# Performance work log

Hardware: AMD Instinct MI355X
Metric: run time of the kernel (lower is better)

## Reference

```python
import jax, jax.numpy as jnp
import numpy as np

N = 2048      # nodes
E = 65536     # edges (avg degree 32)
D_I = 64      # input feature dim
D_O = 64      # output feature dim
EPS = 1e-6


def _one_hot_incidence(key, n, e):
    # each edge column has a single 1 at its endpoint node row -> [N, E]
    idx = jax.random.randint(key, (e,), 0, n)
    return jnp.zeros((n, e), jnp.float32).at[idx, jnp.arange(e)].set(1.0)


def setup_inputs() -> dict:
    key = jax.random.key(0)
    k_x, k_s, k_t, k_wf, k_ww = jax.random.split(key, 5)
    x = jax.random.normal(k_x, (N, D_I), jnp.float32)
    src = _one_hot_incidence(k_s, N, E)
    tgt = _one_hot_incidence(k_t, N, E)
    # xavier-uniform init for Linear(2*d_i, d_o) and Linear(2*d_i, 1)
    lim_f = float(np.sqrt(6.0 / (2 * D_I + D_O)))
    lim_w = float(np.sqrt(6.0 / (2 * D_I + 1)))
    W_f = jax.random.uniform(k_wf, (2 * D_I, D_O), jnp.float32, -lim_f, lim_f)
    b_f = jnp.zeros((D_O,), jnp.float32)
    W_w = jax.random.uniform(k_ww, (2 * D_I, 1), jnp.float32, -lim_w, lim_w)
    b_w = jnp.zeros((1,), jnp.float32)
    return {"x": x, "src": src, "tgt": tgt,
            "W_f": W_f, "b_f": b_f, "W_w": W_w, "b_w": b_w}


def reference(x, src, tgt, W_f, b_f, W_w, b_w):
    # gather source/target node features per edge via dense one-hot matmuls
    hsrc = src.T @ x                      # [E, d_i]
    htgt = tgt.T @ x                      # [E, d_i]
    h = jnp.concatenate([hsrc, htgt], axis=1)   # [E, 2*d_i]
    y = jax.nn.relu(h @ W_f + b_f)        # [E, d_o]
    a = h @ W_w + b_w                     # [E, 1]
    a_max = jnp.mean(a, axis=0, keepdims=True)
    a_exp = jnp.exp(a - a_max)            # [E, 1]
    a_sum = tgt @ a_exp                   # [N, 1] segment-sum over edges per target node
    a_tgt = tgt.T @ a_sum                 # [E, 1] broadcast denominators back to edges
    a_att = a_exp / (a_tgt + EPS)         # edge softmax weights
    o = tgt @ (y * a_att)                 # [N, d_o] weighted scatter-sum
    return o
```

## Files before the change

kernel.cpp:

```cpp
#include <hip/hip_runtime.h>
#include <hip/hip_bf16.h>

#define N_NODES 2048
#define N_EDGES 65536
#define D_IN    64
#define D_OUT   64
#define GAT_EPS 1e-6f

typedef unsigned short u16;
typedef unsigned int   u32;
typedef __attribute__((ext_vector_type(8))) short frag8;
typedef __attribute__((ext_vector_type(4))) float f32x4;

__device__ __forceinline__ u16 f2bf(float f) {
    union { u32 u; float f; } x; x.f = f;
    u32 lsb = (x.u >> 16) & 1u;
    x.u += 0x7fffu + lsb;
    return (u16)(x.u >> 16);
}

__global__ void k_zero2(float* __restrict__ a, int na, float* __restrict__ b, int nb) {
    int i = blockIdx.x * 256 + threadIdx.x;
    if (i < na) a[i] = 0.0f;
    else if (i - na < nb) b[i - na] = 0.0f;
}

__global__ void k_extract2(const uint4* __restrict__ src, const uint4* __restrict__ tgt,
                           int* __restrict__ sidx, int* __restrict__ tidx) {
    u32 b = blockIdx.x;
    const uint4* m; int* idx;
    if (b < 131072u) { m = src; idx = sidx; }
    else             { m = tgt; idx = tidx; b -= 131072u; }
    u32 t = b * 256u + threadIdx.x;
    uint4 v = m[t];
    if (v.x | v.y | v.z | v.w) {
        u32 elem = t * 4u;
        int n = (int)(elem >> 16);
        int e = (int)(elem & 65535u);
        if (v.x) idx[e]     = n;
        if (v.y) idx[e + 1] = n;
        if (v.z) idx[e + 2] = n;
        if (v.w) idx[e + 3] = n;
    }
}

__global__ void k_edge_score(const float* __restrict__ x,
                             const int* __restrict__ sidx, const int* __restrict__ tidx,
                             const float* __restrict__ Ww, const float* __restrict__ bw,
                             float* __restrict__ a, float* __restrict__ mean_acc) {
    __shared__ float ww[2 * D_IN];
    int tid = threadIdx.x;
    if (tid < 2 * D_IN) ww[tid] = Ww[tid];
    __syncthreads();
    int e = blockIdx.x * 256 + tid;
    int s = sidx[e] & (N_NODES - 1);
    int t = tidx[e] & (N_NODES - 1);
    const float4* xs = (const float4*)(x + s * D_IN);
    const float4* xt = (const float4*)(x + t * D_IN);
    float sum = bw[0];
    #pragma unroll
    for (int i = 0; i < 16; ++i) {
        float4 v = xs[i];
        sum += v.x * ww[i * 4] + v.y * ww[i * 4 + 1]
             + v.z * ww[i * 4 + 2] + v.w * ww[i * 4 + 3];
    }
    #pragma unroll
    for (int i = 0; i < 16; ++i) {
        float4 v = xt[i];
        sum += v.x * ww[D_IN + i * 4] + v.y * ww[D_IN + i * 4 + 1]
             + v.z * ww[D_IN + i * 4 + 2] + v.w * ww[D_IN + i * 4 + 3];
    }
    a[e] = sum;
    float r = sum;
    #pragma unroll
    for (int off = 32; off; off >>= 1) r += __shfl_down(r, off);
    if ((tid & 63) == 0) atomicAdd(mean_acc, r);
}

__global__ void k_softmax_prep(const float* __restrict__ a, const int* __restrict__ tidx,
                               const float* __restrict__ mean_acc,
                               float* __restrict__ a_exp, float* __restrict__ a_sum) {
    int e = blockIdx.x * 256 + threadIdx.x;
    float mean = mean_acc[0] * (1.0f / (float)N_EDGES);
    float ae = expf(a[e] - mean);
    a_exp[e] = ae;
    atomicAdd(&a_sum[tidx[e] & (N_NODES - 1)], ae);
}

__global__ void __launch_bounds__(256) k_gemm_scatter(
        const float* __restrict__ x,
        const int* __restrict__ sidx, const int* __restrict__ tidx,
        const float* __restrict__ Wf, const float* __restrict__ bf,
        const float* __restrict__ a_exp, const float* __restrict__ a_sum,
        float* __restrict__ out) {
    __shared__ u16 wt[D_OUT * 2 * D_IN];
    int tid = threadIdx.x;
    for (int i = tid; i < 2 * D_IN * D_OUT; i += 256) {
        int k = i >> 6, d = i & 63;
        wt[d * 128 + k] = f2bf(Wf[i]);
    }
    __syncthreads();

    int wave = tid >> 6, lane = tid & 63;
    int q = lane >> 4, r = lane & 15;
    int e0 = blockIdx.x * 64 + wave * 16;

    int s_r = sidx[e0 + r] & (N_NODES - 1);
    int t_r = tidx[e0 + r] & (N_NODES - 1);
    const float* xs = x + s_r * D_IN;
    const float* xt = x + t_r * D_IN;
    frag8 afr[4];
    #pragma unroll
    for (int c = 0; c < 4; ++c) {
        const float* base = (c < 2 ? xs : xt) + (c & 1) * 32 + q * 8;
        float4 lo = *(const float4*)(base);
        float4 hi = *(const float4*)(base + 4);
        frag8 f;
        f[0] = (short)f2bf(lo.x); f[1] = (short)f2bf(lo.y);
        f[2] = (short)f2bf(lo.z); f[3] = (short)f2bf(lo.w);
        f[4] = (short)f2bf(hi.x); f[5] = (short)f2bf(hi.y);
        f[6] = (short)f2bf(hi.z); f[7] = (short)f2bf(hi.w);
        afr[c] = f;
    }

    f32x4 acc[4] = { {0,0,0,0}, {0,0,0,0}, {0,0,0,0}, {0,0,0,0} };
    #pragma unroll
    for (int c = 0; c < 4; ++c) {
        #pragma unroll
        for (int dt = 0; dt < 4; ++dt) {
            frag8 bfr = *(const frag8*)(&wt[(dt * 16 + r) * 128 + c * 32 + q * 8]);
            acc[dt] = __builtin_amdgcn_mfma_f32_16x16x32_bf16(afr[c], bfr, acc[dt], 0, 0, 0);
        }
    }

    float wgt[4]; int tg[4];
    #pragma unroll
    for (int reg = 0; reg < 4; ++reg) {
        int e = e0 + q * 4 + reg;
        int tt = tidx[e] & (N_NODES - 1);
        tg[reg] = tt;
        wgt[reg] = a_exp[e] / (a_sum[tt] + GAT_EPS);
    }
    #pragma unroll
    for (int dt = 0; dt < 4; ++dt) {
        int d = dt * 16 + r;
        float bias = bf[d];
        #pragma unroll
        for (int reg = 0; reg < 4; ++reg) {
            float y = acc[dt][reg] + bias;
            y = y > 0.0f ? y : 0.0f;
            atomicAdd(&out[tg[reg] * D_OUT + d], y * wgt[reg]);
        }
    }
}

extern "C" void kernel_launch(void* const* d_in, const int* in_sizes, int n_in,
                              void* d_out, int out_size, void* d_ws, size_t ws_size,
                              hipStream_t stream) {
    const float* x   = (const float*)d_in[0];
    const float* src = (const float*)d_in[1];
    const float* tgt = (const float*)d_in[2];
    const float* Wf  = (const float*)d_in[3];
    const float* bf  = (const float*)d_in[4];
    const float* Ww  = (const float*)d_in[5];
    const float* bw  = (const float*)d_in[6];
    float* out = (float*)d_out;

    char* ws = (char*)d_ws;
    float* mean_acc = (float*)(ws);
    float* a_sum    = (float*)(ws + 16);
    int*   sidx     = (int*)  (ws + 16 + 2048 * 4);
    int*   tidx     = (int*)  (ws + 8208 + 262144);
    float* a        = (float*)(ws + 8208 + 2 * 262144);
    float* a_exp    = (float*)(ws + 8208 + 3 * 262144);

    const int n_zero_ws  = 4 + 2048;
    const int n_zero_out = N_NODES * D_OUT;
    k_zero2<<<(n_zero_ws + n_zero_out + 255) / 256, 256, 0, stream>>>(
        (float*)ws, n_zero_ws, out, n_zero_out);
    k_extract2<<<262144, 256, 0, stream>>>((const uint4*)src, (const uint4*)tgt, sidx, tidx);
    k_edge_score<<<N_EDGES / 256, 256, 0, stream>>>(x, sidx, tidx, Ww, bw, a, mean_acc);
    k_softmax_prep<<<N_EDGES / 256, 256, 0, stream>>>(a, tidx, mean_acc, a_exp, a_sum);
    k_gemm_scatter<<<N_EDGES / 64, 256, 0, stream>>>(x, sidx, tidx, Wf, bf, a_exp, a_sum, out);
}
```

Before: 1.000 ms.

## Fuse edge scoring into GEMM scatter, defer softmax normalization to a per-node pass

Edge attention scores are now computed inside the MFMA gather/scatter kernel from the same loaded x rows. The mean shift is dropped because it cancels in the softmax. Unnormalized weighted outputs are accumulated per node, and a small final kernel divides by the per-node exp-sum. That removes the a/a_exp buffers and two separate kernels. The incidence-matrix extract kernel becomes a grid-stride loop with far fewer blocks and also zeroes the workspace, which removes the zero kernel. Without the mean shift, exp could overflow for large scores, and the extract kernel's memory parallelism per block changes.

```diff
diff --git a/kernel.cpp b/kernel.cpp
--- a/kernel.cpp
+++ b/kernel.cpp
@@ -19,82 +19,45 @@
     return (u16)(x.u >> 16);
 }
 
-__global__ void k_zero2(float* __restrict__ a, int na, float* __restrict__ b, int nb) {
-    int i = blockIdx.x * 256 + threadIdx.x;
-    if (i < na) a[i] = 0.0f;
-    else if (i - na < nb) b[i - na] = 0.0f;
-}
-
-__global__ void k_extract2(const uint4* __restrict__ src, const uint4* __restrict__ tgt,
-                           int* __restrict__ sidx, int* __restrict__ tidx) {
-    u32 b = blockIdx.x;
+__global__ void k_extract(const uint4* __restrict__ src, const uint4* __restrict__ tgt,
+                          int* __restrict__ sidx, int* __restrict__ tidx,
+                          float* __restrict__ zero_base) {
+    u32 b = blockIdx.x, tid = threadIdx.x;
+    if (b < 520u) {
+        u32 zi = b * 256u + tid;
+        if (zi < 133120u) zero_base[zi] = 0.0f;
+    }
     const uint4* m; int* idx;
-    if (b < 131072u) { m = src; idx = sidx; }
-    else             { m = tgt; idx = tidx; b -= 131072u; }
-    u32 t = b * 256u + threadIdx.x;
-    uint4 v = m[t];
-    if (v.x | v.y | v.z | v.w) {
-        u32 elem = t * 4u;
-        int n = (int)(elem >> 16);
-        int e = (int)(elem & 65535u);
-        if (v.x) idx[e]     = n;
-        if (v.y) idx[e + 1] = n;
-        if (v.z) idx[e + 2] = n;
-        if (v.w) idx[e + 3] = n;
+    if (b < 2048u) { m = src; idx = sidx; }
+    else           { m = tgt; idx = tidx; b -= 2048u; }
+    u32 t0 = b * 256u + tid;
+    const u32 S = 524288u;
+    #pragma unroll 4
+    for (u32 it = 0; it < 64u; ++it) {
+        u32 t = t0 + it * S;
+        uint4 v = m[t];
+        if (v.x | v.y | v.z | v.w) {
+            u32 elem = t * 4u;
+            int n = (int)(elem >> 16);
+            int e = (int)(elem & 65535u);
+            if (v.x) idx[e]     = n;
+            if (v.y) idx[e + 1] = n;
+            if (v.z) idx[e + 2] = n;
+            if (v.w) idx[e + 3] = n;
+        }
     }
 }
 
-__global__ void k_edge_score(const float* __restrict__ x,
-                             const int* __restrict__ sidx, const int* __restrict__ tidx,
-                             const float* __restrict__ Ww, const float* __restrict__ bw,
-                             float* __restrict__ a, float* __restrict__ mean_acc) {
+__global__ void __launch_bounds__(256) k_fused(
+        const float* __restrict__ x,
+        const int* __restrict__ sidx, const int* __restrict__ tidx,
+        const float* __restrict__ Wf, const float* __restrict__ bf,
+        const float* __restrict__ Ww, const float* __restrict__ bw,
+        float* __restrict__ a_sum, float* __restrict__ out_acc) {
+    __shared__ u16 wt[D_OUT * 2 * D_IN];
     __shared__ float ww[2 * D_IN];
     int tid = threadIdx.x;
     if (tid < 2 * D_IN) ww[tid] = Ww[tid];
-    __syncthreads();
-    int e = blockIdx.x * 256 + tid;
-    int s = sidx[e] & (N_NODES - 1);
-    int t = tidx[e] & (N_NODES - 1);
-    const float4* xs = (const float4*)(x + s * D_IN);
-    const float4* xt = (const float4*)(x + t * D_IN);
-    float sum = bw[0];
-    #pragma unroll
-    for (int i = 0; i < 16; ++i) {
-        float4 v = xs[i];
-        sum += v.x * ww[i * 4] + v.y * ww[i * 4 + 1]
-             + v.z * ww[i * 4 + 2] + v.w * ww[i * 4 + 3];
-    }
-    #pragma unroll
-    for (int i = 0; i < 16; ++i) {
-        float4 v = xt[i];
-        sum += v.x * ww[D_IN + i * 4] + v.y * ww[D_IN + i * 4 + 1]
-             + v.z * ww[D_IN + i * 4 + 2] + v.w * ww[D_IN + i * 4 + 3];
-    }
-    a[e] = sum;
-    float r = sum;
-    #pragma unroll
-    for (int off = 32; off; off >>= 1) r += __shfl_down(r, off);
-    if ((tid & 63) == 0) atomicAdd(mean_acc, r);
-}
-
-__global__ void k_softmax_prep(const float* __restrict__ a, const int* __restrict__ tidx,
-                               const float* __restrict__ mean_acc,
-                               float* __restrict__ a_exp, float* __restrict__ a_sum) {
-    int e = blockIdx.x * 256 + threadIdx.x;
-    float mean = mean_acc[0] * (1.0f / (float)N_EDGES);
-    float ae = expf(a[e] - mean);
-    a_exp[e] = ae;
-    atomicAdd(&a_sum[tidx[e] & (N_NODES - 1)], ae);
-}
-
-__global__ void __launch_bounds__(256) k_gemm_scatter(
-        const float* __restrict__ x,
-        const int* __restrict__ sidx, const int* __restrict__ tidx,
-        const float* __restrict__ Wf, const float* __restrict__ bf,
-        const float* __restrict__ a_exp, const float* __restrict__ a_sum,
-        float* __restrict__ out) {
-    __shared__ u16 wt[D_OUT * 2 * D_IN];
-    int tid = threadIdx.x;
     for (int i = tid; i < 2 * D_IN * D_OUT; i += 256) {
         int k = i >> 6, d = i & 63;
         wt[d * 128 + k] = f2bf(Wf[i]);
@@ -109,12 +72,19 @@
     int t_r = tidx[e0 + r] & (N_NODES - 1);
     const float* xs = x + s_r * D_IN;
     const float* xt = x + t_r * D_IN;
+
     frag8 afr[4];
+    float part = 0.0f;
     #pragma unroll
     for (int c = 0; c < 4; ++c) {
         const float* base = (c < 2 ? xs : xt) + (c & 1) * 32 + q * 8;
+        int kb = (c >> 1) * 64 + (c & 1) * 32 + q * 8;
         float4 lo = *(const float4*)(base);
         float4 hi = *(const float4*)(base + 4);
+        part += lo.x * ww[kb]     + lo.y * ww[kb + 1]
+              + lo.z * ww[kb + 2] + lo.w * ww[kb + 3]
+              + hi.x * ww[kb + 4] + hi.y * ww[kb + 5]
+              + hi.z * ww[kb + 6] + hi.w * ww[kb + 7];
         frag8 f;
         f[0] = (short)f2bf(lo.x); f[1] = (short)f2bf(lo.y);
         f[2] = (short)f2bf(lo.z); f[3] = (short)f2bf(lo.w);
@@ -122,6 +92,10 @@
         f[6] = (short)f2bf(hi.z); f[7] = (short)f2bf(hi.w);
         afr[c] = f;
     }
+    part += __shfl_xor(part, 16);
+    part += __shfl_xor(part, 32);
+    float ae = expf(part + bw[0]);
+    if (lane < 16) atomicAdd(&a_sum[t_r], ae);
 
     f32x4 acc[4] = { {0,0,0,0}, {0,0,0,0}, {0,0,0,0}, {0,0,0,0} };
     #pragma unroll
@@ -133,25 +107,24 @@
         }
     }
 
-    float wgt[4]; int tg[4];
     #pragma unroll
     for (int reg = 0; reg < 4; ++reg) {
-        int e = e0 + q * 4 + reg;
-        int tt = tidx[e] & (N_NODES - 1);
-        tg[reg] = tt;
-        wgt[reg] = a_exp[e] / (a_sum[tt] + GAT_EPS);
-    }
-    #pragma unroll
-    for (int dt = 0; dt < 4; ++dt) {
-        int d = dt * 16 + r;
-        float bias = bf[d];
+        float w  = __shfl(ae,  q * 4 + reg);
+        int   tg = __shfl(t_r, q * 4 + reg);
         #pragma unroll
-        for (int reg = 0; reg < 4; ++reg) {
-            float y = acc[dt][reg] + bias;
+        for (int dt = 0; dt < 4; ++dt) {
+            int d = dt * 16 + r;
+            float y = acc[dt][reg] + bf[d];
             y = y > 0.0f ? y : 0.0f;
-            atomicAdd(&out[tg[reg] * D_OUT + d], y * wgt[reg]);
+            atomicAdd(&out_acc[tg * D_OUT + d], y * w);
         }
     }
+}
+
+__global__ void k_norm(const float* __restrict__ out_acc, const float* __restrict__ a_sum,
+                       float* __restrict__ out) {
+    int i = blockIdx.x * 256 + threadIdx.x;
+    out[i] = out_acc[i] / (a_sum[i >> 6] + GAT_EPS);
 }
 
 extern "C" void kernel_launch(void* const* d_in, const int* in_sizes, int n_in,
@@ -167,19 +140,14 @@
     float* out = (float*)d_out;
 
     char* ws = (char*)d_ws;
-    float* mean_acc = (float*)(ws);
-    float* a_sum    = (float*)(ws + 16);
-    int*   sidx     = (int*)  (ws + 16 + 2048 * 4);
-    int*   tidx     = (int*)  (ws + 8208 + 262144);
-    float* a        = (float*)(ws + 8208 + 2 * 262144);
-    float* a_exp    = (float*)(ws + 8208 + 3 * 262144);
+    float* a_sum   = (float*)(ws);
+    float* out_acc = (float*)(ws + 8192);
+    int*   sidx    = (int*)  (ws + 8192 + 524288);
+    int*   tidx    = (int*)  (ws + 532480 + 262144);
 
-    const int n_zero_ws  = 4 + 2048;
-    const int n_zero_out = N_NODES * D_OUT;
-    k_zero2<<<(n_zero_ws + n_zero_out + 255) / 256, 256, 0, stream>>>(
-        (float*)ws, n_zero_ws, out, n_zero_out);
-    k_extract2<<<262144, 256, 0, stream>>>((const uint4*)src, (const uint4*)tgt, sidx, tidx);
-    k_edge_score<<<N_EDGES / 256, 256, 0, stream>>>(x, sidx, tidx, Ww, bw, a, mean_acc);
-    k_softmax_prep<<<N_EDGES / 256, 256, 0, stream>>>(a, tidx, mean_acc, a_exp, a_sum);
-    k_gemm_scatter<<<N_EDGES / 64, 256, 0, stream>>>(x, sidx, tidx, Wf, bf, a_exp, a_sum, out);
+    k_extract<<<4096, 256, 0, stream>>>((const uint4*)src, (const uint4*)tgt,
+                                        sidx, tidx, (float*)ws);
+    k_fused<<<N_EDGES / 64, 256, 0, stream>>>(x, sidx, tidx, Wf, bf, Ww, bw,
+                                              a_sum, out_acc);
+    k_norm<<<(N_NODES * D_OUT) / 256, 256, 0, stream>>>(out_acc, a_sum, out);
 }
```

After: 997.0 us. Within noise of the previous version (-0.3%).
